# Kernel tuning notes

Measured on AMD Instinct MI355X. Metric: run time of the kernel, lower is better.

The kernel has to match this reference:

```python
import jax, jax.numpy as jnp
import numpy as np

B, NL, C, H, W = 4, 2048, 128, 128, 128
N_PTS0, N_PTS1 = 32, 8
SCALE = N_PTS0 // N_PTS1  # MaxPool1d kernel/stride
FEATURE_DIM = 5
BN_EPS = 1e-5


def setup_inputs() -> dict:
    key = jax.random.key(0)
    ks = jax.random.split(key, 12)
    fm = jax.random.normal(ks[0], (B, C, H, W), dtype=jnp.float32)
    lines = jax.random.uniform(ks[1], (B, NL, 2, 2), dtype=jnp.float32) * 128.0
    P = C // 2
    s = 0.05
    return {
        "feature_map": fm,
        "lines": lines,
        # Bottleneck1D params (BatchNorm in eval mode: running_mean=0, running_var=1)
        "bn1_g": jnp.ones((C,), jnp.float32), "bn1_b": jnp.zeros((C,), jnp.float32),
        "conv1_w": jax.random.normal(ks[2], (P, C, 1), jnp.float32) * s,
        "conv1_b": jnp.zeros((P,), jnp.float32),
        "bn2_g": jnp.ones((P,), jnp.float32), "bn2_b": jnp.zeros((P,), jnp.float32),
        "conv2_w": jax.random.normal(ks[3], (P, P, 3), jnp.float32) * s,
        "conv2_b": jnp.zeros((P,), jnp.float32),
        "bn3_g": jnp.ones((P,), jnp.float32), "bn3_b": jnp.zeros((P,), jnp.float32),
        "conv3_w": jax.random.normal(ks[4], (C, P, 1), jnp.float32) * s,
        "conv3_b": jnp.zeros((C,), jnp.float32),
        # fc2: ReLU -> Linear(dim_loi*n_pts1 + 5, 4)
        "fc2_w": jax.random.normal(ks[5], (4, C * N_PTS1 + FEATURE_DIM), jnp.float32) * s,
        "fc2_b": jnp.zeros((4,), jnp.float32),
    }


def _bn(x, g, b):
    # eval-mode BatchNorm1d with running_mean=0, running_var=1
    return x * (g / jnp.sqrt(1.0 + BN_EPS))[None, :, None] + b[None, :, None]


def _conv1d(x, w, b, pad):
    y = jax.lax.conv_general_dilated(x, w, (1,), [(pad, pad)],
                                     dimension_numbers=("NCH", "OIH", "NCH"))
    return y + b[None, :, None]


def _loi_gather(fm, lines):
    # sample points along each line: [B, NL, N_PTS0, 2]
    lam = jnp.linspace(0.0, 1.0, N_PTS0, dtype=jnp.float32)[None, None, :, None]
    p = lines[:, :, 0:1, :] * lam + lines[:, :, 1:2, :] * (1.0 - lam) - 0.5
    p = p.reshape(B, -1, 2)                      # [B, NL*N_PTS0, 2]
    px, py = p[..., 0], p[..., 1]
    px0 = jnp.clip(jnp.floor(px), 0.0, 127.0)
    py0 = jnp.clip(jnp.floor(py), 0.0, 127.0)
    px1 = jnp.clip(px0 + 1.0, 0.0, 127.0)
    py1 = jnp.clip(py0 + 1.0, 0.0, 127.0)
    px0l, py0l = px0.astype(jnp.int32), py0.astype(jnp.int32)
    px1l, py1l = px1.astype(jnp.int32), py1.astype(jnp.int32)

    gather = jax.vmap(lambda f, yi, xi: f[:, yi, xi])  # [C, P] per image
    # weights exactly as in the torch source
    xp = (gather(fm, py0l, px0l) * ((px1 - px) * (py1 - py))[:, None, :]
          + gather(fm, py1l, px0l) * ((px - px0) * (py1 - py))[:, None, :]
          + gather(fm, py0l, px1l) * ((px1 - px) * (py - py0))[:, None, :]
          + gather(fm, py1l, px1l) * ((px - px0) * (py - py0))[:, None, :])
    # [B, C, NL*N_PTS0] -> [B*NL, C, N_PTS0]
    xp = xp.reshape(B, C, NL, N_PTS0).transpose(0, 2, 1, 3).reshape(B * NL, C, N_PTS0)
    return xp


def reference(feature_map, lines, bn1_g, bn1_b, conv1_w, conv1_b,
              bn2_g, bn2_b, conv2_w, conv2_b, bn3_g, bn3_b,
              conv3_w, conv3_b, fc2_w, fc2_b):
    xp = _loi_gather(feature_map, lines)               # [B*NL, C, N_PTS0]
    # MaxPool1d(SCALE, SCALE)
    x = xp.reshape(B * NL, C, N_PTS1, SCALE).max(axis=-1)
    # Bottleneck1D residual block
    y = jax.nn.relu(_bn(x, bn1_g, bn1_b))
    y = _conv1d(y, conv1_w, conv1_b, 0)
    y = jax.nn.relu(_bn(y, bn2_g, bn2_b))
    y = _conv1d(y, conv2_w, conv2_b, 1)
    y = jax.nn.relu(_bn(y, bn3_g, bn3_b))
    y = _conv1d(y, conv3_w, conv3_b, 0)
    x = x + y                                          # [B*NL, C, N_PTS1]
    # line geometry feature (use_cood=1, use_slop=1)
    xyu, xyv = lines[:, :, 0, :], lines[:, :, 1, :]
    u2v = jnp.sqrt(((xyu - xyv) ** 2).sum(-1, keepdims=True)).clip(min=1e-6)
    f = jnp.concatenate([xyu / 128.0, xyv / 128.0, u2v], axis=-1)
    f = f.reshape(B * NL, FEATURE_DIM)
    # concat + fc2 (ReLU -> Linear)
    x = jnp.concatenate([x.reshape(B * NL, C * N_PTS1), f], axis=1)
    logits = jax.nn.relu(x) @ fc2_w.T + fc2_b
    prob = jax.nn.softmax(logits, axis=1)
    return logits, prob
```

## Files before the change

### kernel.cpp

```cpp
#include <hip/hip_runtime.h>
#include <math.h>

#define BB 4
#define NLL 2048
#define CC 128
#define HH 128
#define WW 128
#define NPTS0 32
#define NPTS1 8
#define PP 64
#define FDIM 5
#define FCK (CC*NPTS1 + FDIM)
#define FCKP 1032

typedef __attribute__((ext_vector_type(8))) short bf16x8;
typedef __attribute__((ext_vector_type(4))) float f32x4;

__device__ __forceinline__ unsigned short f2bf(float f) {
    union { float f; unsigned u; } v; v.f = f;
    unsigned u = v.u;
    return (unsigned short)((u + 0x7fffu + ((u >> 16) & 1u)) >> 16);
}
__device__ __forceinline__ float bf2f(unsigned short s) {
    union { unsigned u; float f; } v; v.u = ((unsigned)s) << 16;
    return v.f;
}

__global__ __launch_bounds__(256)
void transpose_prep(const float* __restrict__ fm, const float* __restrict__ w1,
                    const float* __restrict__ w2, const float* __restrict__ w3,
                    const float* __restrict__ fcw,
                    unsigned short* __restrict__ fmT,
                    unsigned short* __restrict__ W1b,
                    unsigned short* __restrict__ W2b,
                    unsigned short* __restrict__ W3b,
                    float* __restrict__ fcwP) {
    const int t = threadIdx.x;
    if (blockIdx.x >= 512) {
        int gid = (blockIdx.x - 512) * 256 + t;
        for (int e = gid; e < 32800; e += 4096) {
            if (e < 8192) {
                W1b[e] = f2bf(w1[e]);
            } else if (e < 20480) {
                int g = e - 8192;
                int tt = g >> 12, r = g & 4095;
                int p = r >> 6, q = r & 63;
                W2b[tt * 4096 + p * 64 + q] = f2bf(w2[p * 192 + q * 3 + tt]);
            } else if (e < 28672) {
                int g = e - 20480;
                W3b[g] = f2bf(w3[g]);
            } else {
                int g = e - 28672;
                int o = g / FCKP, r = g - o * FCKP;
                fcwP[g] = (r < FCK) ? fcw[o * FCK + r] : 0.0f;
            }
        }
        return;
    }
    __shared__ unsigned short tile[2][128 * 72];
    const int by = blockIdx.x;
    const int b = by >> 7, y = by & 127;
    const float* src = fm + ((size_t)b * CC) * (HH * WW) + (size_t)y * WW;
    const int x4 = (t & 31) * 4;
    const int xh = x4 >> 6, xl = x4 & 63;
    #pragma unroll
    for (int i = 0; i < 16; ++i) {
        int r = (t >> 5) + 8 * i;
        float4 v = *(const float4*)&src[(size_t)r * (HH * WW) + x4];
        ushort4 u;
        u.x = f2bf(v.x); u.y = f2bf(v.y); u.z = f2bf(v.z); u.w = f2bf(v.w);
        *(ushort4*)&tile[xh][r * 72 + (xl ^ (r & 28))] = u;
    }
    __syncthreads();
    const int c4 = (t & 31) * 4;
    #pragma unroll
    for (int h = 0; h < 2; ++h) {
        unsigned short* dst = fmT + ((size_t)by * WW + h * 64) * CC;
        #pragma unroll
        for (int i = 0; i < 8; ++i) {
            int x = (t >> 5) + 8 * i;
            ushort4 u;
            u.x = tile[h][(c4 + 0) * 72 + (x ^ ((c4 + 0) & 28))];
            u.y = tile[h][(c4 + 1) * 72 + (x ^ ((c4 + 1) & 28))];
            u.z = tile[h][(c4 + 2) * 72 + (x ^ ((c4 + 2) & 28))];
            u.w = tile[h][(c4 + 3) * 72 + (x ^ ((c4 + 3) & 28))];
            *(ushort4*)&dst[(size_t)x * CC + c4] = u;
        }
    }
}

__global__ __launch_bounds__(256, 4)
void line_mfma(const unsigned short* __restrict__ fmT,
               const float* __restrict__ lines,
               const float* __restrict__ bn1_g, const float* __restrict__ bn1_b,
               const unsigned short* __restrict__ W1b, const float* __restrict__ b1,
               const float* __restrict__ bn2_g, const float* __restrict__ bn2_b,
               const unsigned short* __restrict__ W2b, const float* __restrict__ b2,
               const float* __restrict__ bn3_g, const float* __restrict__ bn3_b,
               const unsigned short* __restrict__ W3b, const float* __restrict__ b3,
               const float* __restrict__ fcwP,  const float* __restrict__ fcb,
               float* __restrict__ out) {
    __shared__ int   s_oA[64], s_oB[64], s_oC[64], s_oD[64];
    __shared__ float s_wA[64], s_wB[64], s_wC[64], s_wD[64];
    __shared__ float s_xs[16 * 132];
    __shared__ unsigned short s_ybn[16 * 136];
    __shared__ unsigned short s_z1[2 * 10 * 72];
    __shared__ unsigned short s_z2[16 * 72];
    __shared__ float s_feat[2][8];
    __shared__ float s_red[4 * 8];

    const int bx  = blockIdx.x;
    const int L0  = bx * 2;
    const int b   = bx >> 10;
    const int tid = threadIdx.x;
    const int lane = tid & 63;
    const int wv   = tid >> 6;
    const int quad = lane >> 4;
    const int l16  = lane & 15;
    const float inv_s = 1.0f / sqrtf(1.0f + 1e-5f);

    if (tid < 64) {
        int line = tid >> 5, pt = tid & 31;
        const float* ln = lines + (size_t)(L0 + line) * 4;
        float lam = (float)pt * (1.0f / 31.0f);
        float om  = 1.0f - lam;
        float px = ln[0] * lam + ln[2] * om - 0.5f;
        float py = ln[1] * lam + ln[3] * om - 0.5f;
        float px0 = fminf(fmaxf(floorf(px), 0.0f), 127.0f);
        float py0 = fminf(fmaxf(floorf(py), 0.0f), 127.0f);
        float px1 = fminf(px0 + 1.0f, 127.0f);
        float py1 = fminf(py0 + 1.0f, 127.0f);
        int ix0 = (int)px0, ix1 = (int)px1, iy0 = (int)py0, iy1 = (int)py1;
        s_oA[tid] = (iy0 * WW + ix0) * CC;
        s_oB[tid] = (iy1 * WW + ix0) * CC;
        s_oC[tid] = (iy0 * WW + ix1) * CC;
        s_oD[tid] = (iy1 * WW + ix1) * CC;
        float ax = px1 - px, bxv = px - px0, ay = py1 - py, byv = py - py0;
        s_wA[tid] = ax  * ay;
        s_wB[tid] = bxv * ay;
        s_wC[tid] = ax  * byv;
        s_wD[tid] = bxv * byv;
    }
    if (tid >= 64 && tid < 66) {
        int line = tid - 64;
        const float* ln = lines + (size_t)(L0 + line) * 4;
        float ux = ln[0], uy = ln[1], vx = ln[2], vy = ln[3];
        float dx = ux - vx, dy = uy - vy;
        float d = fmaxf(sqrtf(dx * dx + dy * dy), 1e-6f);
        s_feat[line][0] = ux * (1.0f / 128.0f);
        s_feat[line][1] = uy * (1.0f / 128.0f);
        s_feat[line][2] = vx * (1.0f / 128.0f);
        s_feat[line][3] = vy * (1.0f / 128.0f);
        s_feat[line][4] = d;
    }
    if (tid < 128) {
        int line = tid >> 6, q = tid & 63;
        s_z1[line * 720 + 0 * 72 + q] = 0;
        s_z1[line * 720 + 9 * 72 + q] = 0;
    }
    __syncthreads();

    {
        int tl = tid >> 4;
        int line = tl >> 3, k = tl & 7;
        int c8 = (tid & 15) * 8;
        const unsigned short* base = fmT + (size_t)b * (HH * WW * CC) + c8;
        const int pts = line * 32 + k * 4;
        bf16x8 rA[4], rB[4], rC[4], rD[4];
        #pragma unroll
        for (int j = 0; j < 4; ++j) {
            rA[j] = *(const bf16x8*)(base + s_oA[pts + j]);
            rB[j] = *(const bf16x8*)(base + s_oB[pts + j]);
            rC[j] = *(const bf16x8*)(base + s_oC[pts + j]);
            rD[j] = *(const bf16x8*)(base + s_oD[pts + j]);
        }
        float acc[8];
        #pragma unroll
        for (int i = 0; i < 8; ++i) acc[i] = -INFINITY;
        #pragma unroll
        for (int j = 0; j < 4; ++j) {
            float wA = s_wA[pts + j], wB = s_wB[pts + j];
            float wC = s_wC[pts + j], wD = s_wD[pts + j];
            #pragma unroll
            for (int i = 0; i < 8; ++i) {
                float v = wA * bf2f((unsigned short)rA[j][i])
                        + wB * bf2f((unsigned short)rB[j][i])
                        + wC * bf2f((unsigned short)rC[j][i])
                        + wD * bf2f((unsigned short)rD[j][i]);
                acc[i] = fmaxf(acc[i], v);
            }
        }
        float* xr = &s_xs[tl * 132 + c8];
        f32x4 lo = {acc[0], acc[1], acc[2], acc[3]};
        f32x4 hi = {acc[4], acc[5], acc[6], acc[7]};
        *(f32x4*)&xr[0] = lo;
        *(f32x4*)&xr[4] = hi;
        bf16x8 pack;
        #pragma unroll
        for (int i = 0; i < 8; ++i) {
            float v = fmaxf(acc[i] * (bn1_g[c8 + i] * inv_s) + bn1_b[c8 + i], 0.0f);
            pack[i] = (short)f2bf(v);
        }
        *(bf16x8*)&s_ybn[tl * 136 + c8] = pack;
    }
    __syncthreads();

    {
        int n0 = wv * 16;
        f32x4 acc = {0.f, 0.f, 0.f, 0.f};
        #pragma unroll
        for (int kc = 0; kc < 4; ++kc) {
            bf16x8 a = *(const bf16x8*)&s_ybn[l16 * 136 + kc * 32 + quad * 8];
            bf16x8 bf = *(const bf16x8*)(W1b + (n0 + l16) * 128 + kc * 32 + quad * 8);
            acc = __builtin_amdgcn_mfma_f32_16x16x32_bf16(a, bf, acc, 0, 0, 0);
        }
        int p = n0 + l16;
        float s2 = bn2_g[p] * inv_s, bb2 = bn2_b[p], cb = b1[p];
        int line = quad >> 1;
        int kbase = (quad & 1) * 4;
        #pragma unroll
        for (int r = 0; r < 4; ++r) {
            float v = fmaxf((acc[r] + cb) * s2 + bb2, 0.0f);
            s_z1[line * 720 + (kbase + r + 1) * 72 + p] = f2bf(v);
        }
    }
    __syncthreads();

    {
        int n0 = wv * 16;
        f32x4 acc = {0.f, 0.f, 0.f, 0.f};
        int line = l16 >> 3, k = l16 & 7;
        #pragma unroll
        for (int t = 0; t < 3; ++t) {
            const unsigned short* arow = &s_z1[line * 720 + (k + t) * 72];
            #pragma unroll
            for (int kc = 0; kc < 2; ++kc) {
                bf16x8 a = *(const bf16x8*)&arow[kc * 32 + quad * 8];
                bf16x8 bf = *(const bf16x8*)(W2b + t * 4096 + (n0 + l16) * 64 + kc * 32 + quad * 8);
                acc = __builtin_amdgcn_mfma_f32_16x16x32_bf16(a, bf, acc, 0, 0, 0);
            }
        }
        int p = n0 + l16;
        float s3 = bn3_g[p] * inv_s, bb3 = bn3_b[p], cb = b2[p];
        #pragma unroll
        for (int r = 0; r < 4; ++r) {
            float v = fmaxf((acc[r] + cb) * s3 + bb3, 0.0f);
            s_z2[(quad * 4 + r) * 72 + p] = f2bf(v);
        }
    }
    __syncthreads();

    float p0 = 0.f, p1 = 0.f, p2 = 0.f, p3 = 0.f;
    {
        int kbase = (quad & 1) * 4;
        bf16x8 a0 = *(const bf16x8*)&s_z2[l16 * 72 + 0 * 32 + quad * 8];
        bf16x8 a1 = *(const bf16x8*)&s_z2[l16 * 72 + 1 * 32 + quad * 8];
        #pragma unroll
        for (int sub = 0; sub < 2; ++sub) {
            int n0 = wv * 32 + sub * 16;
            f32x4 acc = {0.f, 0.f, 0.f, 0.f};
            bf16x8 bf0 = *(const bf16x8*)(W3b + (n0 + l16) * 64 + 0 * 32 + quad * 8);
            bf16x8 bf1 = *(const bf16x8*)(W3b + (n0 + l16) * 64 + 1 * 32 + quad * 8);
            acc = __builtin_amdgcn_mfma_f32_16x16x32_bf16(a0, bf0, acc, 0, 0, 0);
            acc = __builtin_amdgcn_mfma_f32_16x16x32_bf16(a1, bf1, acc, 0, 0, 0);
            int c = n0 + l16;
            float cb = b3[c];
            int idx = c * 8 + kbase;
            float4 w0 = *(const float4*)(fcwP + 0 * FCKP + idx);
            float4 w1v = *(const float4*)(fcwP + 1 * FCKP + idx);
            float4 w2v = *(const float4*)(fcwP + 2 * FCKP + idx);
            float4 w3v = *(const float4*)(fcwP + 3 * FCKP + idx);
            const float* w0a = (const float*)&w0;
            const float* w1a = (const float*)&w1v;
            const float* w2a = (const float*)&w2v;
            const float* w3a = (const float*)&w3v;
            #pragma unroll
            for (int r = 0; r < 4; ++r) {
                int m = quad * 4 + r;
                float v = fmaxf(s_xs[m * 132 + c] + acc[r] + cb, 0.0f);
                p0 = fmaf(v, w0a[r], p0);
                p1 = fmaf(v, w1a[r], p1);
                p2 = fmaf(v, w2a[r], p2);
                p3 = fmaf(v, w3a[r], p3);
            }
        }
    }
    #pragma unroll
    for (int off = 16; off >= 1; off >>= 1) {
        p0 += __shfl_down(p0, off);
        p1 += __shfl_down(p1, off);
        p2 += __shfl_down(p2, off);
        p3 += __shfl_down(p3, off);
    }
    if ((lane & 31) == 0) {
        int line = lane >> 5;
        s_red[wv * 8 + line * 4 + 0] = p0;
        s_red[wv * 8 + line * 4 + 1] = p1;
        s_red[wv * 8 + line * 4 + 2] = p2;
        s_red[wv * 8 + line * 4 + 3] = p3;
    }
    __syncthreads();

    if (tid < 2) {
        int line = tid;
        float lg[4];
        #pragma unroll
        for (int o = 0; o < 4; ++o) {
            lg[o] = fcb[o] + s_red[0 + line * 4 + o] + s_red[8 + line * 4 + o]
                  + s_red[16 + line * 4 + o] + s_red[24 + line * 4 + o];
        }
        #pragma unroll
        for (int j = 0; j < FDIM; ++j) {
            float fv = fmaxf(s_feat[line][j], 0.0f);
            #pragma unroll
            for (int o = 0; o < 4; ++o)
                lg[o] = fmaf(fv, fcwP[o * FCKP + 1024 + j], lg[o]);
        }
        float m = fmaxf(fmaxf(lg[0], lg[1]), fmaxf(lg[2], lg[3]));
        float e0 = expf(lg[0] - m), e1 = expf(lg[1] - m);
        float e2 = expf(lg[2] - m), e3 = expf(lg[3] - m);
        float inv = 1.0f / (e0 + e1 + e2 + e3);
        float* lo = out + (size_t)(L0 + line) * 4;
        lo[0] = lg[0]; lo[1] = lg[1]; lo[2] = lg[2]; lo[3] = lg[3];
        float* pr = out + (size_t)BB * NLL * 4 + (size_t)(L0 + line) * 4;
        pr[0] = e0 * inv; pr[1] = e1 * inv; pr[2] = e2 * inv; pr[3] = e3 * inv;
    }
}

__global__ __launch_bounds__(256)
void transpose_fm2(const float* __restrict__ fm, float* __restrict__ fmT) {
    __shared__ float tile[32 * 132];
    const int c0 = blockIdx.x * 32;
    const int by = blockIdx.y;
    const int b = by >> 7, y = by & 127;
    const int t = threadIdx.x;
    const float* src = fm + ((size_t)b * CC) * (HH * WW) + (size_t)y * WW;
    const int x4 = (t & 31) * 4;
    #pragma unroll
    for (int i = 0; i < 4; ++i) {
        int r = (t >> 5) + 8 * i;
        *(float4*)&tile[r * 132 + x4] =
            *(const float4*)&src[(size_t)(c0 + r) * (HH * WW) + x4];
    }
    __syncthreads();
    float* dst = fmT + (size_t)by * WW * CC + c0 + (t & 31);
    const int cr = (t & 31) * 132;
    #pragma unroll
    for (int i = 0; i < 16; ++i) {
        int x = (t >> 5) + 8 * i;
        dst[(size_t)x * CC] = tile[cr + x];
    }
}

template<bool TRANS>
__global__ __launch_bounds__(256)
void line_kernel_v1(const float* __restrict__ fm,
                    const float* __restrict__ lines,
                    const float* __restrict__ bn1_g, const float* __restrict__ bn1_b,
                    const float* __restrict__ w1,    const float* __restrict__ b1,
                    const float* __restrict__ bn2_g, const float* __restrict__ bn2_b,
                    const float* __restrict__ w2,    const float* __restrict__ b2,
                    const float* __restrict__ bn3_g, const float* __restrict__ bn3_b,
                    const float* __restrict__ w3,    const float* __restrict__ b3,
                    const float* __restrict__ fcw,   const float* __restrict__ fcb,
                    float* __restrict__ out) {
    __shared__ int   s_ix0[32], s_ix1[32], s_iy0[32], s_iy1[32];
    __shared__ float s_wA[32], s_wB[32], s_wC[32], s_wD[32];
    __shared__ float xs [8][132];
    __shared__ float ybn[8][132];
    __shared__ float z1 [64][12];
    __shared__ float z2 [64][8];
    __shared__ float s_feat[8];
    __shared__ float s_red[16];

    const int L   = blockIdx.x;
    const int b   = L / NLL;
    const int tid = threadIdx.x;
    const float inv_s = 1.0f / sqrtf(1.0f + 1e-5f);
    const float* ln = lines + (size_t)L * 4;

    if (tid < 32) {
        float lam = (float)tid * (1.0f / 31.0f);
        float om  = 1.0f - lam;
        float px = ln[0] * lam + ln[2] * om - 0.5f;
        float py = ln[1] * lam + ln[3] * om - 0.5f;
        float px0 = fminf(fmaxf(floorf(px), 0.0f), 127.0f);
        float py0 = fminf(fmaxf(floorf(py), 0.0f), 127.0f);
        float px1 = fminf(px0 + 1.0f, 127.0f);
        float py1 = fminf(py0 + 1.0f, 127.0f);
        s_ix0[tid] = (int)px0; s_ix1[tid] = (int)px1;
        s_iy0[tid] = (int)py0; s_iy1[tid] = (int)py1;
        float ax = px1 - px, bxv = px - px0, ay = py1 - py, byv = py - py0;
        s_wA[tid] = ax  * ay;  s_wB[tid] = bxv * ay;
        s_wC[tid] = ax  * byv; s_wD[tid] = bxv * byv;
    }
    if (tid == 0) {
        float ux = ln[0], uy = ln[1], vx = ln[2], vy = ln[3];
        float dx = ux - vx, dy = uy - vy;
        float d = fmaxf(sqrtf(dx * dx + dy * dy), 1e-6f);
        s_feat[0] = ux / 128.0f; s_feat[1] = uy / 128.0f;
        s_feat[2] = vx / 128.0f; s_feat[3] = vy / 128.0f;
        s_feat[4] = d;
    }
    __syncthreads();
    {
        int cq = tid & 31, k = tid >> 5, c0 = cq * 4;
        float4 acc;
        acc.x = -INFINITY; acc.y = -INFINITY; acc.z = -INFINITY; acc.w = -INFINITY;
        #pragma unroll
        for (int j = 0; j < 4; ++j) {
            int pt = k * 4 + j;
            int ix0 = s_ix0[pt], ix1 = s_ix1[pt];
            int iy0 = s_iy0[pt], iy1 = s_iy1[pt];
            float wA = s_wA[pt], wB = s_wB[pt], wC = s_wC[pt], wD = s_wD[pt];
            float4 vA, vB, vC, vD;
            if (TRANS) {
                const float* base = fm + (size_t)b * HH * WW * CC;
                vA = *(const float4*)(base + ((size_t)(iy0 * WW + ix0)) * CC + c0);
                vB = *(const float4*)(base + ((size_t)(iy1 * WW + ix0)) * CC + c0);
                vC = *(const float4*)(base + ((size_t)(iy0 * WW + ix1)) * CC + c0);
                vD = *(const float4*)(base + ((size_t)(iy1 * WW + ix1)) * CC + c0);
            } else {
                const float* base = fm + ((size_t)b * CC + c0) * HH * WW;
                int oA = iy0 * WW + ix0, oB = iy1 * WW + ix0;
                int oC = iy0 * WW + ix1, oD = iy1 * WW + ix1;
                vA.x = base[oA];           vB.x = base[oB];
                vC.x = base[oC];           vD.x = base[oD];
                vA.y = base[HH*WW + oA];   vB.y = base[HH*WW + oB];
                vC.y = base[HH*WW + oC];   vD.y = base[HH*WW + oD];
                vA.z = base[2*HH*WW + oA]; vB.z = base[2*HH*WW + oB];
                vC.z = base[2*HH*WW + oC]; vD.z = base[2*HH*WW + oD];
                vA.w = base[3*HH*WW + oA]; vB.w = base[3*HH*WW + oB];
                vC.w = base[3*HH*WW + oC]; vD.w = base[3*HH*WW + oD];
            }
            float4 v;
            v.x = wA * vA.x + wB * vB.x + wC * vC.x + wD * vD.x;
            v.y = wA * vA.y + wB * vB.y + wC * vC.y + wD * vD.y;
            v.z = wA * vA.z + wB * vB.z + wC * vC.z + wD * vD.z;
            v.w = wA * vA.w + wB * vB.w + wC * vC.w + wD * vD.w;
            acc.x = fmaxf(acc.x, v.x); acc.y = fmaxf(acc.y, v.y);
            acc.z = fmaxf(acc.z, v.z); acc.w = fmaxf(acc.w, v.w);
        }
        *(float4*)(&xs[k][c0]) = acc;
    }
    __syncthreads();
    for (int e = tid; e < 1024; e += 256) {
        int k = e >> 7, c = e & 127;
        ybn[k][c] = fmaxf(xs[k][c] * (bn1_g[c] * inv_s) + bn1_b[c], 0.0f);
    }
    __syncthreads();
    if (tid < 64) { z1[tid][0] = 0.0f; z1[tid][9] = 0.0f; }
    {
        int p = tid >> 2, kq = tid & 3;
        const float* wrow = w1 + p * 128;
        float a0a = 0.f, a0b = 0.f, a1a = 0.f, a1b = 0.f;
        #pragma unroll 8
        for (int c = 0; c < 128; c += 4) {
            float4 w  = *(const float4*)(wrow + c);
            float4 ya = *(const float4*)(&ybn[kq][c]);
            float4 yb = *(const float4*)(&ybn[kq + 4][c]);
            a0a = fmaf(w.x, ya.x, a0a); a0b = fmaf(w.y, ya.y, a0b);
            a0a = fmaf(w.z, ya.z, a0a); a0b = fmaf(w.w, ya.w, a0b);
            a1a = fmaf(w.x, yb.x, a1a); a1b = fmaf(w.y, yb.y, a1b);
            a1a = fmaf(w.z, yb.z, a1a); a1b = fmaf(w.w, yb.w, a1b);
        }
        float s2 = bn2_g[p] * inv_s, bb = bn2_b[p], cb = b1[p];
        z1[p][1 + kq]     = fmaxf((a0a + a0b + cb) * s2 + bb, 0.0f);
        z1[p][1 + kq + 4] = fmaxf((a1a + a1b + cb) * s2 + bb, 0.0f);
    }
    __syncthreads();
    {
        int p = tid >> 2, kq = tid & 3;
        const float* wrow = w2 + p * 192;
        float acc0 = 0.f, acc1 = 0.f;
        #pragma unroll 4
        for (int q = 0; q < 64; ++q) {
            float w0 = wrow[q * 3 + 0], w1v = wrow[q * 3 + 1], w2v = wrow[q * 3 + 2];
            const float* zr = &z1[q][0];
            acc0 = fmaf(w0, zr[kq], acc0);
            acc0 = fmaf(w1v, zr[kq + 1], acc0);
            acc0 = fmaf(w2v, zr[kq + 2], acc0);
            acc1 = fmaf(w0, zr[kq + 4], acc1);
            acc1 = fmaf(w1v, zr[kq + 5], acc1);
            acc1 = fmaf(w2v, zr[kq + 6], acc1);
        }
        float s3 = bn3_g[p] * inv_s, bb = bn3_b[p], cb = b2[p];
        z2[p][kq]     = fmaxf((acc0 + cb) * s3 + bb, 0.0f);
        z2[p][kq + 4] = fmaxf((acc1 + cb) * s3 + bb, 0.0f);
    }
    __syncthreads();
    float part0 = 0.f, part1 = 0.f, part2 = 0.f, part3 = 0.f;
    {
        int c = tid >> 1, kq = tid & 1;
        const float* wrow = w3 + c * 64;
        float acc[4] = {0.f, 0.f, 0.f, 0.f};
        #pragma unroll 8
        for (int q = 0; q < 64; ++q) {
            float w = wrow[q];
            acc[0] = fmaf(w, z2[q][kq], acc[0]);
            acc[1] = fmaf(w, z2[q][kq + 2], acc[1]);
            acc[2] = fmaf(w, z2[q][kq + 4], acc[2]);
            acc[3] = fmaf(w, z2[q][kq + 6], acc[3]);
        }
        float cb = b3[c];
        #pragma unroll
        for (int i = 0; i < 4; ++i) {
            int k = kq + 2 * i;
            float v = fmaxf(xs[k][c] + acc[i] + cb, 0.0f);
            int idx = c * 8 + k;
            part0 = fmaf(v, fcw[0 * FCK + idx], part0);
            part1 = fmaf(v, fcw[1 * FCK + idx], part1);
            part2 = fmaf(v, fcw[2 * FCK + idx], part2);
            part3 = fmaf(v, fcw[3 * FCK + idx], part3);
        }
    }
    #pragma unroll
    for (int off = 32; off > 0; off >>= 1) {
        part0 += __shfl_down(part0, off);
        part1 += __shfl_down(part1, off);
        part2 += __shfl_down(part2, off);
        part3 += __shfl_down(part3, off);
    }
    if ((tid & 63) == 0) {
        int w = tid >> 6;
        s_red[w * 4 + 0] = part0; s_red[w * 4 + 1] = part1;
        s_red[w * 4 + 2] = part2; s_red[w * 4 + 3] = part3;
    }
    __syncthreads();
    if (tid == 0) {
        float lg[4];
        #pragma unroll
        for (int o = 0; o < 4; ++o)
            lg[o] = fcb[o] + s_red[o] + s_red[4 + o] + s_red[8 + o] + s_red[12 + o];
        #pragma unroll
        for (int j = 0; j < FDIM; ++j) {
            float fv = fmaxf(s_feat[j], 0.0f);
            #pragma unroll
            for (int o = 0; o < 4; ++o)
                lg[o] = fmaf(fv, fcw[o * FCK + 1024 + j], lg[o]);
        }
        float m = fmaxf(fmaxf(lg[0], lg[1]), fmaxf(lg[2], lg[3]));
        float e0 = expf(lg[0] - m), e1 = expf(lg[1] - m);
        float e2 = expf(lg[2] - m), e3 = expf(lg[3] - m);
        float inv = 1.0f / (e0 + e1 + e2 + e3);
        float* lo = out + (size_t)L * 4;
        lo[0] = lg[0]; lo[1] = lg[1]; lo[2] = lg[2]; lo[3] = lg[3];
        float* pr = out + (size_t)BB * NLL * 4 + (size_t)L * 4;
        pr[0] = e0 * inv; pr[1] = e1 * inv; pr[2] = e2 * inv; pr[3] = e3 * inv;
    }
}

extern "C" void kernel_launch(void* const* d_in, const int* in_sizes, int n_in,
                              void* d_out, int out_size, void* d_ws, size_t ws_size,
                              hipStream_t stream) {
    const float* fm     = (const float*)d_in[0];
    const float* lines  = (const float*)d_in[1];
    const float* bn1_g  = (const float*)d_in[2];
    const float* bn1_b  = (const float*)d_in[3];
    const float* w1     = (const float*)d_in[4];
    const float* b1     = (const float*)d_in[5];
    const float* bn2_g  = (const float*)d_in[6];
    const float* bn2_b  = (const float*)d_in[7];
    const float* w2     = (const float*)d_in[8];
    const float* b2     = (const float*)d_in[9];
    const float* bn3_g  = (const float*)d_in[10];
    const float* bn3_b  = (const float*)d_in[11];
    const float* w3     = (const float*)d_in[12];
    const float* b3     = (const float*)d_in[13];
    const float* fcw    = (const float*)d_in[14];
    const float* fcb    = (const float*)d_in[15];
    float* out = (float*)d_out;

    const size_t fmTb_bytes = (size_t)BB * HH * WW * CC * sizeof(unsigned short);
    const size_t fmTf_bytes = (size_t)BB * HH * WW * CC * sizeof(float);
    const size_t wb_bytes   = 57344;
    const size_t fcwP_bytes = 4 * FCKP * sizeof(float);

    if (ws_size >= fmTb_bytes + wb_bytes + fcwP_bytes) {
        unsigned short* fmT = (unsigned short*)d_ws;
        unsigned short* W1b = (unsigned short*)((char*)d_ws + fmTb_bytes);
        unsigned short* W2b = W1b + 8192;
        unsigned short* W3b = W2b + 12288;
        float* fcwP = (float*)((char*)d_ws + fmTb_bytes + wb_bytes);
        transpose_prep<<<512 + 16, 256, 0, stream>>>(
            fm, w1, w2, w3, fcw, fmT, W1b, W2b, W3b, fcwP);
        line_mfma<<<BB * NLL / 2, 256, 0, stream>>>(
            fmT, lines, bn1_g, bn1_b, W1b, b1, bn2_g, bn2_b, W2b, b2,
            bn3_g, bn3_b, W3b, b3, fcwP, fcb, out);
    } else if (ws_size >= fmTf_bytes) {
        float* fmT = (float*)d_ws;
        dim3 tg(CC / 32, BB * HH);
        transpose_fm2<<<tg, 256, 0, stream>>>(fm, fmT);
        line_kernel_v1<true><<<BB * NLL, 256, 0, stream>>>(
            fmT, lines, bn1_g, bn1_b, w1, b1, bn2_g, bn2_b, w2, b2,
            bn3_g, bn3_b, w3, b3, fcw, fcb, out);
    } else {
        line_kernel_v1<false><<<BB * NLL, 256, 0, stream>>>(
            fm, lines, bn1_g, bn1_b, w1, b1, bn2_g, bn2_b, w2, b2,
            bn3_g, bn3_b, w3, b3, fcw, fcb, out);
    }
}
```

Before: 150.5 us.

## Split fused line kernel into gather kernel and batched conv/FC MFMA kernel

The fused per-2-line kernel is split into a gather_xs kernel that bilinearly samples, max-pools and applies BN1+ReLU, writing bf16 activations to workspace, and a conv_fc kernel that processes 8 lines per block with full 16-row MFMA tiles for all three convolutions plus the FC head. This aims to improve MFMA utilisation and weight reuse per block and to shrink per-block shared memory. In exchange it adds a global round trip for two intermediate bf16 buffers and one extra launch. The new path only runs when the workspace is large enough; the fp32-transpose fallback path is removed.

```diff
diff --git a/kernel.cpp b/kernel.cpp
--- a/kernel.cpp
+++ b/kernel.cpp
@@ -90,33 +90,18 @@
 }
 
 __global__ __launch_bounds__(256, 4)
-void line_mfma(const unsigned short* __restrict__ fmT,
+void gather_xs(const unsigned short* __restrict__ fmT,
                const float* __restrict__ lines,
                const float* __restrict__ bn1_g, const float* __restrict__ bn1_b,
-               const unsigned short* __restrict__ W1b, const float* __restrict__ b1,
-               const float* __restrict__ bn2_g, const float* __restrict__ bn2_b,
-               const unsigned short* __restrict__ W2b, const float* __restrict__ b2,
-               const float* __restrict__ bn3_g, const float* __restrict__ bn3_b,
-               const unsigned short* __restrict__ W3b, const float* __restrict__ b3,
-               const float* __restrict__ fcwP,  const float* __restrict__ fcb,
-               float* __restrict__ out) {
+               unsigned short* __restrict__ xs_g,
+               unsigned short* __restrict__ ybn_g) {
     __shared__ int   s_oA[64], s_oB[64], s_oC[64], s_oD[64];
     __shared__ float s_wA[64], s_wB[64], s_wC[64], s_wD[64];
-    __shared__ float s_xs[16 * 132];
-    __shared__ unsigned short s_ybn[16 * 136];
-    __shared__ unsigned short s_z1[2 * 10 * 72];
-    __shared__ unsigned short s_z2[16 * 72];
-    __shared__ float s_feat[2][8];
-    __shared__ float s_red[4 * 8];
 
     const int bx  = blockIdx.x;
     const int L0  = bx * 2;
     const int b   = bx >> 10;
     const int tid = threadIdx.x;
-    const int lane = tid & 63;
-    const int wv   = tid >> 6;
-    const int quad = lane >> 4;
-    const int l16  = lane & 15;
     const float inv_s = 1.0f / sqrtf(1.0f + 1e-5f);
 
     if (tid < 64) {
@@ -141,6 +126,263 @@
         s_wC[tid] = ax  * byv;
         s_wD[tid] = bxv * byv;
     }
+    __syncthreads();
+
+    {
+        int tl = tid >> 4;
+        int line = tl >> 3, k = tl & 7;
+        int c8 = (tid & 15) * 8;
+        const unsigned short* base = fmT + (size_t)b * (HH * WW * CC) + c8;
+        const int pts = line * 32 + k * 4;
+        bf16x8 rA[4], rB[4], rC[4], rD[4];
+        #pragma unroll
+        for (int j = 0; j < 4; ++j) {
+            rA[j] = *(const bf16x8*)(base + s_oA[pts + j]);
+            rB[j] = *(const bf16x8*)(base + s_oB[pts + j]);
+            rC[j] = *(const bf16x8*)(base + s_oC[pts + j]);
+            rD[j] = *(const bf16x8*)(base + s_oD[pts + j]);
+        }
+        float acc[8];
+        #pragma unroll
+        for (int i = 0; i < 8; ++i) acc[i] = -INFINITY;
+        #pragma unroll
+        for (int j = 0; j < 4; ++j) {
+            float wA = s_wA[pts + j], wB = s_wB[pts + j];
+            float wC = s_wC[pts + j], wD = s_wD[pts + j];
+            #pragma unroll
+            for (int i = 0; i < 8; ++i) {
+                float v = wA * bf2f((unsigned short)rA[j][i])
+                        + wB * bf2f((unsigned short)rB[j][i])
+                        + wC * bf2f((unsigned short)rC[j][i])
+                        + wD * bf2f((unsigned short)rD[j][i]);
+                acc[i] = fmaxf(acc[i], v);
+            }
+        }
+        size_t row = (size_t)L0 * 8 + tl;
+        bf16x8 pkx, pky;
+        #pragma unroll
+        for (int i = 0; i < 8; ++i) {
+            pkx[i] = (short)f2bf(acc[i]);
+            float v = fmaxf(acc[i] * (bn1_g[c8 + i] * inv_s) + bn1_b[c8 + i], 0.0f);
+            pky[i] = (short)f2bf(v);
+        }
+        *(bf16x8*)(xs_g  + row * 128 + c8) = pkx;
+        *(bf16x8*)(ybn_g + row * 128 + c8) = pky;
+    }
+}
+
+__global__ __launch_bounds__(256, 4)
+void conv_fc(const unsigned short* __restrict__ xs_g,
+             const unsigned short* __restrict__ ybn_g,
+             const float* __restrict__ lines,
+             const unsigned short* __restrict__ W1b, const float* __restrict__ b1,
+             const float* __restrict__ bn2_g, const float* __restrict__ bn2_b,
+             const unsigned short* __restrict__ W2b, const float* __restrict__ b2,
+             const float* __restrict__ bn3_g, const float* __restrict__ bn3_b,
+             const unsigned short* __restrict__ W3b, const float* __restrict__ b3,
+             const float* __restrict__ fcwP,  const float* __restrict__ fcb,
+             float* __restrict__ out) {
+    __shared__ unsigned short s_z1[8 * 10 * 72];
+    __shared__ unsigned short s_z2[64 * 72];
+
+    const int bx  = blockIdx.x;
+    const int G0  = bx * 8;
+    const int tid = threadIdx.x;
+    const int lane = tid & 63;
+    const int wv   = tid >> 6;
+    const int quad = lane >> 4;
+    const int l16  = lane & 15;
+    const float inv_s = 1.0f / sqrtf(1.0f + 1e-5f);
+    const size_t rbase = (size_t)G0 * 8;
+
+    for (int e = tid; e < 1024; e += 256) {
+        int lline = e >> 7;
+        int rr = (e >> 6) & 1;
+        int q = e & 63;
+        s_z1[lline * 720 + (rr ? 9 : 0) * 72 + q] = 0;
+    }
+
+    {
+        bf16x8 afr[4];
+        #pragma unroll
+        for (int kc = 0; kc < 4; ++kc)
+            afr[kc] = *(const bf16x8*)(ybn_g + (rbase + wv * 16 + l16) * 128
+                                       + kc * 32 + quad * 8);
+        #pragma unroll
+        for (int sub = 0; sub < 4; ++sub) {
+            int p = sub * 16 + l16;
+            f32x4 acc = {0.f, 0.f, 0.f, 0.f};
+            #pragma unroll
+            for (int kc = 0; kc < 4; ++kc) {
+                bf16x8 bf = *(const bf16x8*)(W1b + p * 128 + kc * 32 + quad * 8);
+                acc = __builtin_amdgcn_mfma_f32_16x16x32_bf16(afr[kc], bf, acc, 0, 0, 0);
+            }
+            float s2 = bn2_g[p] * inv_s, bb2 = bn2_b[p], cb = b1[p];
+            #pragma unroll
+            for (int r = 0; r < 4; ++r) {
+                int m = wv * 16 + quad * 4 + r;
+                int lline = m >> 3, kk = m & 7;
+                float v = fmaxf((acc[r] + cb) * s2 + bb2, 0.0f);
+                s_z1[lline * 720 + (kk + 1) * 72 + p] = f2bf(v);
+            }
+        }
+    }
+    __syncthreads();
+
+    {
+        int m = wv * 16 + l16;
+        int linea = m >> 3, ka = m & 7;
+        const unsigned short* arow = s_z1 + linea * 720 + ka * 72;
+        bf16x8 afr[3][2];
+        #pragma unroll
+        for (int t = 0; t < 3; ++t)
+            #pragma unroll
+            for (int kc = 0; kc < 2; ++kc)
+                afr[t][kc] = *(const bf16x8*)&arow[t * 72 + kc * 32 + quad * 8];
+        #pragma unroll
+        for (int sub = 0; sub < 4; ++sub) {
+            int p = sub * 16 + l16;
+            f32x4 acc = {0.f, 0.f, 0.f, 0.f};
+            #pragma unroll
+            for (int t = 0; t < 3; ++t) {
+                #pragma unroll
+                for (int kc = 0; kc < 2; ++kc) {
+                    bf16x8 bf = *(const bf16x8*)(W2b + t * 4096 + p * 64 + kc * 32 + quad * 8);
+                    acc = __builtin_amdgcn_mfma_f32_16x16x32_bf16(afr[t][kc], bf, acc, 0, 0, 0);
+                }
+            }
+            float s3 = bn3_g[p] * inv_s, bb3 = bn3_b[p], cb = b2[p];
+            #pragma unroll
+            for (int r = 0; r < 4; ++r) {
+                int m2 = wv * 16 + quad * 4 + r;
+                float v = fmaxf((acc[r] + cb) * s3 + bb3, 0.0f);
+                s_z2[m2 * 72 + p] = f2bf(v);
+            }
+        }
+    }
+    __syncthreads();
+
+    float p0 = 0.f, p1 = 0.f, p2 = 0.f, p3 = 0.f;
+    {
+        int kbase = (quad & 1) * 4;
+        bf16x8 a0 = *(const bf16x8*)&s_z2[(wv * 16 + l16) * 72 + quad * 8];
+        bf16x8 a1 = *(const bf16x8*)&s_z2[(wv * 16 + l16) * 72 + 32 + quad * 8];
+        #pragma unroll
+        for (int sub = 0; sub < 8; ++sub) {
+            int c = sub * 16 + l16;
+            f32x4 acc = {0.f, 0.f, 0.f, 0.f};
+            bf16x8 bf0 = *(const bf16x8*)(W3b + c * 64 + quad * 8);
+            bf16x8 bf1 = *(const bf16x8*)(W3b + c * 64 + 32 + quad * 8);
+            acc = __builtin_amdgcn_mfma_f32_16x16x32_bf16(a0, bf0, acc, 0, 0, 0);
+            acc = __builtin_amdgcn_mfma_f32_16x16x32_bf16(a1, bf1, acc, 0, 0, 0);
+            float cb = b3[c];
+            int idx = c * 8 + kbase;
+            float4 w0 = *(const float4*)(fcwP + 0 * FCKP + idx);
+            float4 w1v = *(const float4*)(fcwP + 1 * FCKP + idx);
+            float4 w2v = *(const float4*)(fcwP + 2 * FCKP + idx);
+            float4 w3v = *(const float4*)(fcwP + 3 * FCKP + idx);
+            const float* w0a = (const float*)&w0;
+            const float* w1a = (const float*)&w1v;
+            const float* w2a = (const float*)&w2v;
+            const float* w3a = (const float*)&w3v;
+            #pragma unroll
+            for (int r = 0; r < 4; ++r) {
+                int m = wv * 16 + quad * 4 + r;
+                float xv = bf2f(xs_g[(rbase + m) * 128 + c]);
+                float v = fmaxf(xv + acc[r] + cb, 0.0f);
+                p0 = fmaf(v, w0a[r], p0);
+                p1 = fmaf(v, w1a[r], p1);
+                p2 = fmaf(v, w2a[r], p2);
+                p3 = fmaf(v, w3a[r], p3);
+            }
+        }
+    }
+    #pragma unroll
+    for (int off = 16; off >= 1; off >>= 1) {
+        p0 += __shfl_down(p0, off);
+        p1 += __shfl_down(p1, off);
+        p2 += __shfl_down(p2, off);
+        p3 += __shfl_down(p3, off);
+    }
+    if ((lane & 31) == 0) {
+        int gl = G0 + wv * 2 + (lane >> 5);
+        float lg[4] = {fcb[0] + p0, fcb[1] + p1, fcb[2] + p2, fcb[3] + p3};
+        const float* ln = lines + (size_t)gl * 4;
+        float ux = ln[0], uy = ln[1], vx = ln[2], vy = ln[3];
+        float dx = ux - vx, dy = uy - vy;
+        float d = fmaxf(sqrtf(dx * dx + dy * dy), 1e-6f);
+        float ft[FDIM] = {ux * (1.0f / 128.0f), uy * (1.0f / 128.0f),
+                          vx * (1.0f / 128.0f), vy * (1.0f / 128.0f), d};
+        #pragma unroll
+        for (int j = 0; j < FDIM; ++j) {
+            float fv = fmaxf(ft[j], 0.0f);
+            #pragma unroll
+            for (int o = 0; o < 4; ++o)
+                lg[o] = fmaf(fv, fcwP[o * FCKP + 1024 + j], lg[o]);
+        }
+        float m = fmaxf(fmaxf(lg[0], lg[1]), fmaxf(lg[2], lg[3]));
+        float e0 = expf(lg[0] - m), e1 = expf(lg[1] - m);
+        float e2 = expf(lg[2] - m), e3 = expf(lg[3] - m);
+        float inv = 1.0f / (e0 + e1 + e2 + e3);
+        float4 lo = {lg[0], lg[1], lg[2], lg[3]};
+        float4 pr = {e0 * inv, e1 * inv, e2 * inv, e3 * inv};
+        *(float4*)(out + (size_t)gl * 4) = lo;
+        *(float4*)(out + (size_t)BB * NLL * 4 + (size_t)gl * 4) = pr;
+    }
+}
+
+__global__ __launch_bounds__(256, 4)
+void line_mfma(const unsigned short* __restrict__ fmT,
+               const float* __restrict__ lines,
+               const float* __restrict__ bn1_g, const float* __restrict__ bn1_b,
+               const unsigned short* __restrict__ W1b, const float* __restrict__ b1,
+               const float* __restrict__ bn2_g, const float* __restrict__ bn2_b,
+               const unsigned short* __restrict__ W2b, const float* __restrict__ b2,
+               const float* __restrict__ bn3_g, const float* __restrict__ bn3_b,
+               const unsigned short* __restrict__ W3b, const float* __restrict__ b3,
+               const float* __restrict__ fcwP,  const float* __restrict__ fcb,
+               float* __restrict__ out) {
+    __shared__ int   s_oA[64], s_oB[64], s_oC[64], s_oD[64];
+    __shared__ float s_wA[64], s_wB[64], s_wC[64], s_wD[64];
+    __shared__ float s_xs[16 * 132];
+    __shared__ unsigned short s_ybn[16 * 136];
+    __shared__ unsigned short s_z1[2 * 10 * 72];
+    __shared__ unsigned short s_z2[16 * 72];
+    __shared__ float s_feat[2][8];
+    __shared__ float s_red[4 * 8];
+
+    const int bx  = blockIdx.x;
+    const int L0  = bx * 2;
+    const int b   = bx >> 10;
+    const int tid = threadIdx.x;
+    const int lane = tid & 63;
+    const int wv   = tid >> 6;
+    const int quad = lane >> 4;
+    const int l16  = lane & 15;
+    const float inv_s = 1.0f / sqrtf(1.0f + 1e-5f);
+
+    if (tid < 64) {
+        int line = tid >> 5, pt = tid & 31;
+        const float* ln = lines + (size_t)(L0 + line) * 4;
+        float lam = (float)pt * (1.0f / 31.0f);
+        float om  = 1.0f - lam;
+        float px = ln[0] * lam + ln[2] * om - 0.5f;
+        float py = ln[1] * lam + ln[3] * om - 0.5f;
+        float px0 = fminf(fmaxf(floorf(px), 0.0f), 127.0f);
+        float py0 = fminf(fmaxf(floorf(py), 0.0f), 127.0f);
+        float px1 = fminf(px0 + 1.0f, 127.0f);
+        float py1 = fminf(py0 + 1.0f, 127.0f);
+        int ix0 = (int)px0, ix1 = (int)px1, iy0 = (int)py0, iy1 = (int)py1;
+        s_oA[tid] = (iy0 * WW + ix0) * CC;
+        s_oB[tid] = (iy1 * WW + ix0) * CC;
+        s_oC[tid] = (iy0 * WW + ix1) * CC;
+        s_oD[tid] = (iy1 * WW + ix1) * CC;
+        float ax = px1 - px, bxv = px - px0, ay = py1 - py, byv = py - py0;
+        s_wA[tid] = ax  * ay;
+        s_wB[tid] = bxv * ay;
+        s_wC[tid] = ax  * byv;
+        s_wD[tid] = bxv * byv;
+    }
     if (tid >= 64 && tid < 66) {
         int line = tid - 64;
         const float* ln = lines + (size_t)(L0 + line) * 4;
@@ -324,31 +566,6 @@
         lo[0] = lg[0]; lo[1] = lg[1]; lo[2] = lg[2]; lo[3] = lg[3];
         float* pr = out + (size_t)BB * NLL * 4 + (size_t)(L0 + line) * 4;
         pr[0] = e0 * inv; pr[1] = e1 * inv; pr[2] = e2 * inv; pr[3] = e3 * inv;
-    }
-}
-
-__global__ __launch_bounds__(256)
-void transpose_fm2(const float* __restrict__ fm, float* __restrict__ fmT) {
-    __shared__ float tile[32 * 132];
-    const int c0 = blockIdx.x * 32;
-    const int by = blockIdx.y;
-    const int b = by >> 7, y = by & 127;
-    const int t = threadIdx.x;
-    const float* src = fm + ((size_t)b * CC) * (HH * WW) + (size_t)y * WW;
-    const int x4 = (t & 31) * 4;
-    #pragma unroll
-    for (int i = 0; i < 4; ++i) {
-        int r = (t >> 5) + 8 * i;
-        *(float4*)&tile[r * 132 + x4] =
-            *(const float4*)&src[(size_t)(c0 + r) * (HH * WW) + x4];
-    }
-    __syncthreads();
-    float* dst = fmT + (size_t)by * WW * CC + c0 + (t & 31);
-    const int cr = (t & 31) * 132;
-    #pragma unroll
-    for (int i = 0; i < 16; ++i) {
-        int x = (t >> 5) + 8 * i;
-        dst[(size_t)x * CC] = tile[cr + x];
     }
 }
 
@@ -572,11 +789,13 @@
     float* out = (float*)d_out;
 
     const size_t fmTb_bytes = (size_t)BB * HH * WW * CC * sizeof(unsigned short);
-    const size_t fmTf_bytes = (size_t)BB * HH * WW * CC * sizeof(float);
     const size_t wb_bytes   = 57344;
     const size_t fcwP_bytes = 4 * FCKP * sizeof(float);
-
-    if (ws_size >= fmTb_bytes + wb_bytes + fcwP_bytes) {
+    const size_t xs_bytes   = (size_t)BB * NLL * 8 * 128 * sizeof(unsigned short);
+    const size_t base_bytes  = fmTb_bytes + wb_bytes + fcwP_bytes;
+    const size_t split_bytes = base_bytes + 2 * xs_bytes;
+
+    if (ws_size >= base_bytes) {
         unsigned short* fmT = (unsigned short*)d_ws;
         unsigned short* W1b = (unsigned short*)((char*)d_ws + fmTb_bytes);
         unsigned short* W2b = W1b + 8192;
@@ -584,16 +803,19 @@
         float* fcwP = (float*)((char*)d_ws + fmTb_bytes + wb_bytes);
         transpose_prep<<<512 + 16, 256, 0, stream>>>(
             fm, w1, w2, w3, fcw, fmT, W1b, W2b, W3b, fcwP);
-        line_mfma<<<BB * NLL / 2, 256, 0, stream>>>(
-            fmT, lines, bn1_g, bn1_b, W1b, b1, bn2_g, bn2_b, W2b, b2,
-            bn3_g, bn3_b, W3b, b3, fcwP, fcb, out);
-    } else if (ws_size >= fmTf_bytes) {
-        float* fmT = (float*)d_ws;
-        dim3 tg(CC / 32, BB * HH);
-        transpose_fm2<<<tg, 256, 0, stream>>>(fm, fmT);
-        line_kernel_v1<true><<<BB * NLL, 256, 0, stream>>>(
-            fmT, lines, bn1_g, bn1_b, w1, b1, bn2_g, bn2_b, w2, b2,
-            bn3_g, bn3_b, w3, b3, fcw, fcb, out);
+        if (ws_size >= split_bytes) {
+            unsigned short* xs_g  = (unsigned short*)((char*)d_ws + base_bytes);
+            unsigned short* ybn_g = xs_g + xs_bytes / sizeof(unsigned short);
+            gather_xs<<<BB * NLL / 2, 256, 0, stream>>>(
+                fmT, lines, bn1_g, bn1_b, xs_g, ybn_g);
+            conv_fc<<<BB * NLL / 8, 256, 0, stream>>>(
+                xs_g, ybn_g, lines, W1b, b1, bn2_g, bn2_b, W2b, b2,
+                bn3_g, bn3_b, W3b, b3, fcwP, fcb, out);
+        } else {
+            line_mfma<<<BB * NLL / 2, 256, 0, stream>>>(
+                fmT, lines, bn1_g, bn1_b, W1b, b1, bn2_g, bn2_b, W2b, b2,
+                bn3_g, bn3_b, W3b, b3, fcwP, fcb, out);
+        }
     } else {
         line_kernel_v1<false><<<BB * NLL, 256, 0, stream>>>(
             fm, lines, bn1_g, bn1_b, w1, b1, bn2_g, bn2_b, w2, b2,
```

After: 158.5 us. 5.3% more time.
